# Kernel optimization log

Measured on AMD Instinct MI355X. Metric: run time of the kernel, lower is better.

The kernel has to match this reference:

```python
import jax, jax.numpy as jnp
import numpy as np

ARITY = 8        # children per node (< max_child_number=10, so all children used)
TREE_DEPTH = 5   # internal levels 1..5; depth=5 so GRU applies at every internal node
DIM = 384        # cgf_input_dim == GRU input == GRU hidden (unidirectional, n_layers=1)
VOCAB = 32000


def gru_seq(xs, h0, w_ih, w_hh, b_ih, b_hh):
    # xs: [S, N, D] sequence-major, h0: [N, D]. torch nn.GRU gate order: r, z, n.
    def step(h, x_t):
        gi = x_t @ w_ih.T + b_ih            # [N, 3D]
        gh = h @ w_hh.T + b_hh              # [N, 3D]
        i_r, i_z, i_n = jnp.split(gi, 3, axis=-1)
        h_r, h_z, h_n = jnp.split(gh, 3, axis=-1)
        r = jax.nn.sigmoid(i_r + h_r)
        z = jax.nn.sigmoid(i_z + h_z)
        n = jnp.tanh(i_n + r * h_n)
        h_new = (1.0 - z) * n + z * h
        return h_new, h_new
    h_last, outs = jax.lax.scan(step, h0, xs)
    return outs, h_last                      # [S, N, D], [N, D]


def setup_inputs() -> dict:
    key = jax.random.key(0)
    k1, k2, k3, k4, k5, k6 = jax.random.split(key, 6)
    n_leaves = ARITY ** TREE_DEPTH
    s = 1.0 / np.sqrt(DIM)
    return {
        "leaf_tokens": jax.random.randint(k1, (n_leaves,), 0, VOCAB, dtype=jnp.int32),
        "embed_table": jax.random.normal(k2, (VOCAB, DIM), jnp.float32),
        "w_ih": jax.random.uniform(k3, (3 * DIM, DIM), jnp.float32, -s, s),
        "w_hh": jax.random.uniform(k4, (3 * DIM, DIM), jnp.float32, -s, s),
        "b_ih": jax.random.uniform(k5, (3 * DIM,), jnp.float32, -s, s),
        "b_hh": jax.random.uniform(k6, (3 * DIM,), jnp.float32, -s, s),
    }


def reference(leaf_tokens, embed_table, w_ih, w_hh, b_ih, b_hh):
    # Leaves: embedding-dict lookup -> x=[1,1,D] per leaf; h = zeros.
    x = embed_table[leaf_tokens]             # [A^T, D]
    h = jnp.zeros_like(x)                    # leaf hidden states are zeros
    # Level-synchronous post-order: process deepest internal level first.
    for level in range(TREE_DEPTH, 0, -1):
        n_parents = ARITY ** (level - 1)
        # Children are consumed from last to first (loop i = len-1 .. 0), so
        # the GRU sequence is the REVERSED child order.
        xs = x.reshape(n_parents, ARITY, DIM)[:, ::-1, :].transpose(1, 0, 2)  # [A, P, D]
        h0 = h.reshape(n_parents, ARITY, DIM).mean(axis=1)                     # mean of child hiddens
        outs, h = gru_seq(xs, h0, w_ih, w_hh, b_ih, b_hh)
        x = outs.mean(axis=0)                # mean over the child sequence -> node output [P, D]
    # Root (layer=1) returns res = out of shape [1,1,D]
    return x.reshape(1, 1, DIM)
```

## Files before the change

kernel.cpp:

```cpp
#include <hip/hip_runtime.h>
#include <hip/hip_bf16.h>
#include <stdint.h>

typedef float f32x4 __attribute__((ext_vector_type(4)));
typedef short bf16x8 __attribute__((ext_vector_type(8)));

#define NSLOT 16
#define NDS 24
#define NBLK (NSLOT * NDS)
#define NCTR 788
#define CI(i) ((i) * 32)

__device__ __forceinline__ ushort to_bf16(float f) {
    union { float f; uint32_t u; } v; v.f = f;
    uint32_t u = v.u;
    return (ushort)((u + 0x7fffu + ((u >> 16) & 1u)) >> 16);
}
__device__ __forceinline__ float sigmoid_(float x) { return 1.0f / (1.0f + __expf(-x)); }
__device__ __forceinline__ float tanh_(float x)    { return 1.0f - 2.0f / (__expf(2.0f * x) + 1.0f); }

__device__ __forceinline__ void st_sc1_u16(ushort* p, ushort v) {
    asm volatile("global_store_short %0, %1, off sc1" :: "v"(p), "v"((uint32_t)v) : "memory");
}
__device__ __forceinline__ void st_sc1_f32(float* p, float v) {
    asm volatile("global_store_dword %0, %1, off sc1" :: "v"(p), "v"(v) : "memory");
}
__device__ __forceinline__ void st_sc1_b128(void* p, bf16x8 v) {
    asm volatile("global_store_dwordx4 %0, %1, off sc1" :: "v"(p), "v"(v) : "memory");
}

__global__ void prep_w(const float* __restrict__ w_ih, const float* __restrict__ w_hh,
                       ushort* __restrict__ wswz, unsigned int* __restrict__ ctr) {
    int tid = blockIdx.x * blockDim.x + threadIdx.x;
    if (tid < NCTR * 32) ctr[tid] = 0u;
    if (tid >= 1152 * 96) return;
    int g  = tid / 96;
    int k  = (tid % 96) * 8;
    int kc = k >> 5;
    int q  = (k >> 3) & 3;
    int tile = g >> 4;
    int lane = q * 16 + (g & 15);
    ushort* dst = wswz + ((size_t)(tile * 24 + kc) * 64 + lane) * 8;
    const float* src = (k < 384) ? (w_ih + (size_t)g * 384 + k)
                                 : (w_hh + (size_t)g * 384 + (k - 384));
#pragma unroll
    for (int j = 0; j < 8; ++j) dst[j] = to_bf16(src[j]);
}

__global__ void embed_gather(const int* __restrict__ tok, const float* __restrict__ table,
                             ushort* __restrict__ xleaf, int n_leaves) {
    int tid = blockIdx.x * blockDim.x + threadIdx.x;
    if (tid >= n_leaves * 48) return;
    int leaf = tid / 48, i = tid % 48;
    const float* src = table + (size_t)tok[leaf] * 384 + i * 8;
    bf16x8 v;
#pragma unroll
    for (int j = 0; j < 8; ++j) v[j] = (short)to_bf16(src[j]);
    *(bf16x8*)(xleaf + (size_t)leaf * 384 + i * 8) = v;
}

__device__ __forceinline__ void wait_ge(unsigned int* c, unsigned int n) {
    while (__hip_atomic_fetch_add(c, 0u, __ATOMIC_RELAXED, __HIP_MEMORY_SCOPE_AGENT) < n)
        __builtin_amdgcn_s_sleep(1);
}
__device__ __forceinline__ void wait_ge_coarse(unsigned int* c, unsigned int n) {
    while (__hip_atomic_fetch_add(c, 0u, __ATOMIC_RELAXED, __HIP_MEMORY_SCOPE_AGENT) < n)
        __builtin_amdgcn_s_sleep(127);
}

__device__ __forceinline__ void group_arrive(unsigned int* c) {
    __syncthreads();
    if (threadIdx.x == 0)
        __hip_atomic_fetch_add(c, 1u, __ATOMIC_RELAXED, __HIP_MEMORY_SCOPE_AGENT);
}
__device__ __forceinline__ void group_wait(unsigned int* c) {
    if (threadIdx.x == 0) wait_ge(c, NDS);
    __syncthreads();
}

__device__ __forceinline__ void full_barrier(unsigned int* grpSlot, unsigned int* master) {
    __syncthreads();
    if (threadIdx.x == 0) {
        unsigned int old = __hip_atomic_fetch_add(grpSlot, 1u, __ATOMIC_RELAXED, __HIP_MEMORY_SCOPE_AGENT);
        if (old == NDS - 1)
            __hip_atomic_fetch_add(master, 1u, __ATOMIC_RELAXED, __HIP_MEMORY_SCOPE_AGENT);
        wait_ge_coarse(master, NSLOT);
    }
    __syncthreads();
}

__global__ __launch_bounds__(256, 2)
void tree_gru(const ushort* __restrict__ XA, const ushort* __restrict__ W,
              const float* __restrict__ b_ih, const float* __restrict__ b_hh,
              ushort* __restrict__ HBar, float* __restrict__ Hfar,
              ushort* __restrict__ Xoar,
              unsigned int* __restrict__ ctr, float* __restrict__ out)
{
    __shared__ __align__(16) ushort lw[36864];
    __shared__ __align__(16) ushort stage[4][768];
    const int l = blockIdx.x;
    const int dr = l >> 3;
    const int slot = (l & 7) * 2 + (dr / 24);
    const int ds = dr % 24;
    const int tid = threadIdx.x;
    const int wave = tid >> 6, lane = tid & 63;
    const int quad = lane >> 4, col = lane & 15;
    const int d = ds * 16 + col;

    {
        bf16x8* dstv = (bf16x8*)lw;
#pragma unroll
        for (int g = 0; g < 3; ++g) {
            const bf16x8* s = (const bf16x8*)(W + (size_t)(g * NDS + ds) * 12288);
#pragma unroll
            for (int i = 0; i < 6; ++i) dstv[g * 1536 + i * 256 + tid] = s[i * 256 + tid];
        }
    }
    __syncthreads();

    const float br = b_ih[d] + b_hh[d];
    const float bz = b_ih[384 + d] + b_hh[384 + d];
    const float bi = b_ih[768 + d], bh = b_hh[768 + d];
    const ushort* lwr = &lw[(size_t)lane * 8];

#pragma unroll 1
    for (int lvl = 0; lvl < 5; ++lvl) {
        const int P  = (lvl == 0) ? 4096 : (lvl == 1) ? 512 : (lvl == 2) ? 64 : (lvl == 3) ? 8 : 1;
        const int rp = (lvl == 0) ? 0 : (lvl == 1) ? 4096 : (lvl == 2) ? 4608 : (lvl == 3) ? 4672 : 4680;
        const int rpPrev = (lvl == 1) ? 0 : (lvl == 2) ? 4096 : (lvl == 3) ? 4608 : 4672;
        const int nmp = (P + 31) >> 5;
        const bool leaf = (lvl == 0), root = (lvl == 4);
        const ushort* Xc = leaf ? XA : (Xoar + (size_t)384 * rpPrev);
        const float* Hfprev = leaf ? nullptr : (Hfar + (size_t)384 * rpPrev);
        ushort* HBlvl = HBar + (size_t)9 * 384 * rp;
        ushort* Xout  = Xoar + (size_t)384 * rp;
        float*  Hfout = root ? nullptr : (Hfar + (size_t)384 * rp);
        const size_t N = (size_t)P * 384;
        const bool act = (slot * 4 < nmp);
        if (act) {
            const int mpA = slot * 4 + wave;
            const int mpB = mpA + NSLOT * 4;
            const bool hasA = mpA < nmp;
            const bool hasB = mpB < nmp;
            float hpA[2][4], hsA[2][4], hpB[2][4], hsB[2][4];
#pragma unroll
            for (int mt = 0; mt < 2; ++mt)
#pragma unroll
                for (int r = 0; r < 4; ++r) {
                    hpA[mt][r] = 0.f; hsA[mt][r] = 0.f;
                    hpB[mt][r] = 0.f; hsB[mt][r] = 0.f;
                }
            const f32x4 z4 = (f32x4){0.f, 0.f, 0.f, 0.f};
            const bf16x8 zf = (bf16x8){0, 0, 0, 0, 0, 0, 0, 0};
            struct XA6 { f32x4 r[2], z[2], n[2]; } xA, xB;

            auto xpart = [&](int mp, int child, XA6& o) {
                const int m0 = mp * 32;
                const bool do2 = (m0 + 16) < P;
                const int par0 = m0 + col, par1 = m0 + 16 + col;
                const bool av0 = par0 < P, av1 = par1 < P;
                const ushort* xr0 = Xc + ((size_t)par0 * 8 + child) * 384 + quad * 8;
                const ushort* xr1 = Xc + ((size_t)par1 * 8 + child) * 384 + quad * 8;
                o.r[0] = z4; o.z[0] = z4; o.n[0] = z4;
                o.r[1] = z4; o.z[1] = z4; o.n[1] = z4;
#pragma unroll
                for (int kc = 0; kc < 12; ++kc) {
                    bf16x8 a0 = zf, a1 = zf;
                    if (av0) a0 = *(const bf16x8*)(xr0 + kc * 32);
                    if (do2 && av1) a1 = *(const bf16x8*)(xr1 + kc * 32);
                    bf16x8 bR = *(const bf16x8*)(lwr + kc * 512);
                    bf16x8 bZ = *(const bf16x8*)(lwr + 12288 + kc * 512);
                    bf16x8 bN = *(const bf16x8*)(lwr + 24576 + kc * 512);
                    o.r[0] = __builtin_amdgcn_mfma_f32_16x16x32_bf16(a0, bR, o.r[0], 0, 0, 0);
                    o.z[0] = __builtin_amdgcn_mfma_f32_16x16x32_bf16(a0, bZ, o.z[0], 0, 0, 0);
                    o.n[0] = __builtin_amdgcn_mfma_f32_16x16x32_bf16(a0, bN, o.n[0], 0, 0, 0);
                    if (do2) {
                        o.r[1] = __builtin_amdgcn_mfma_f32_16x16x32_bf16(a1, bR, o.r[1], 0, 0, 0);
                        o.z[1] = __builtin_amdgcn_mfma_f32_16x16x32_bf16(a1, bZ, o.z[1], 0, 0, 0);
                        o.n[1] = __builtin_amdgcn_mfma_f32_16x16x32_bf16(a1, bN, o.n[1], 0, 0, 0);
                    }
                }
            };
            auto prol = [&](int mp, float (&hp)[2][4]) {
                const int m0 = mp * 32;
#pragma unroll
                for (int mt = 0; mt < 2; ++mt)
#pragma unroll
                    for (int r = 0; r < 4; ++r) {
                        const int m = m0 + mt * 16 + quad * 4 + r;
                        if (m < P) {
                            const float* hc = Hfprev + (size_t)m * 8 * 384 + d;
                            float h0 = 0.f;
#pragma unroll
                            for (int c = 0; c < 8; ++c) h0 += hc[(size_t)c * 384];
                            h0 *= 0.125f;
                            hp[mt][r] = h0;
                            st_sc1_u16(&HBlvl[(size_t)m * 384 + d], to_bf16(h0));
                        }
                    }
            };
            auto hpart = [&](int mp, XA6& x, float (&hp)[2][4], float (&hs)[2][4],
                             const ushort* HBp, ushort* HBn, bool hz, bool last) {
                const int m0 = mp * 32;
                const bool do2 = (m0 + 16) < P;
                const int par0 = m0 + col, par1 = m0 + 16 + col;
                const bool av0 = par0 < P, av1 = par1 < P;
                f32x4 n2a = z4, n2b = z4;
                if (!hz) {
                    const ushort* hr0 = HBp + (size_t)par0 * 384 + quad * 8;
                    const ushort* hr1 = HBp + (size_t)par1 * 384 + quad * 8;
#pragma unroll
                    for (int kc = 0; kc < 12; ++kc) {
                        bf16x8 a0 = zf, a1 = zf;
                        if (av0) a0 = *(const bf16x8*)(hr0 + kc * 32);
                        if (do2 && av1) a1 = *(const bf16x8*)(hr1 + kc * 32);
                        bf16x8 bR = *(const bf16x8*)(lwr + (12 + kc) * 512);
                        bf16x8 bZ = *(const bf16x8*)(lwr + 12288 + (12 + kc) * 512);
                        bf16x8 bN = *(const bf16x8*)(lwr + 24576 + (12 + kc) * 512);
                        x.r[0] = __builtin_amdgcn_mfma_f32_16x16x32_bf16(a0, bR, x.r[0], 0, 0, 0);
                        x.z[0] = __builtin_amdgcn_mfma_f32_16x16x32_bf16(a0, bZ, x.z[0], 0, 0, 0);
                        n2a    = __builtin_amdgcn_mfma_f32_16x16x32_bf16(a0, bN, n2a, 0, 0, 0);
                        if (do2) {
                            x.r[1] = __builtin_amdgcn_mfma_f32_16x16x32_bf16(a1, bR, x.r[1], 0, 0, 0);
                            x.z[1] = __builtin_amdgcn_mfma_f32_16x16x32_bf16(a1, bZ, x.z[1], 0, 0, 0);
                            n2b    = __builtin_amdgcn_mfma_f32_16x16x32_bf16(a1, bN, n2b, 0, 0, 0);
                        }
                    }
                }
#pragma unroll
                for (int mt = 0; mt < 2; ++mt) {
                    if (mt && !do2) break;
                    const f32x4 ar = x.r[mt], az = x.z[mt], an1 = x.n[mt];
                    const f32x4 an2 = mt ? n2b : n2a;
#pragma unroll
                    for (int r = 0; r < 4; ++r) {
                        const int m = m0 + mt * 16 + quad * 4 + r;
                        if (m < P) {
                            float rv = sigmoid_(ar[r] + br);
                            float zv = sigmoid_(az[r] + bz);
                            float nv = tanh_(an1[r] + bi + rv * (an2[r] + bh));
                            float hn = (1.0f - zv) * nv + zv * hp[mt][r];
                            hp[mt][r] = hn;
                            hs[mt][r] += hn;
                            if (last) {
                                const size_t idx = (size_t)m * 384 + d;
                                float xo = hs[mt][r] * 0.125f;
                                st_sc1_u16(&Xout[idx], to_bf16(xo));
                                if (!root) st_sc1_f32(&Hfout[idx], hn);
                                else if (m == 0) out[d] = xo;
                            } else {
                                stage[wave][(mt * 16 + quad * 4 + r) * 24 + col] = to_bf16(hn);
                            }
                        }
                    }
                }
                if (!last) {
                    const int row = lane >> 1, half = lane & 1;
                    const int m = m0 + row;
                    if (m < P) {
                        bf16x8 v = *(const bf16x8*)&stage[wave][row * 24 + half * 8];
                        st_sc1_b128(HBn + (size_t)m * 384 + ds * 16 + half * 8, v);
                    }
                }
            };

            if (!leaf) {
                if (hasA) prol(mpA, hpA);
                if (hasB) prol(mpB, hpB);
                group_arrive(&ctr[CI((lvl * 9 + 8) * NSLOT + slot)]);
                if (hasA) xpart(mpA, 7, xA);
                if (hasB) xpart(mpB, 7, xB);
                group_wait(&ctr[CI((lvl * 9 + 8) * NSLOT + slot)]);
            } else {
                if (hasA) xpart(mpA, 7, xA);
                if (hasB) xpart(mpB, 7, xB);
            }
#pragma unroll 1
            for (int t = 0; t < 8; ++t) {
                const ushort* HBp = HBlvl + (size_t)t * N;
                ushort*       HBn = HBlvl + (size_t)(t + 1) * N;
                const bool hz   = leaf && (t == 0);
                const bool last = (t == 7);
                if (hasA) hpart(mpA, xA, hpA, hsA, HBp, HBn, hz, last);
                if (hasB) hpart(mpB, xB, hpB, hsB, HBp, HBn, hz, last);
                if (!last) {
                    unsigned int* c = &ctr[CI((lvl * 9 + t) * NSLOT + slot)];
                    group_arrive(c);
                    const int nchild = 6 - t;
                    if (hasA) xpart(mpA, nchild, xA);
                    if (hasB) xpart(mpB, nchild, xB);
                    group_wait(c);
                }
            }
        }
        if (lvl < 4) full_barrier(&ctr[CI(720 + lvl * NSLOT + slot)], &ctr[CI(784 + lvl)]);
    }
}

extern "C" void kernel_launch(void* const* d_in, const int* in_sizes, int n_in,
                              void* d_out, int out_size, void* d_ws, size_t ws_size,
                              hipStream_t stream) {
    const int*   tok   = (const int*)d_in[0];
    const float* table = (const float*)d_in[1];
    const float* w_ih  = (const float*)d_in[2];
    const float* w_hh  = (const float*)d_in[3];
    const float* b_ih  = (const float*)d_in[4];
    const float* b_hh  = (const float*)d_in[5];
    float* out = (float*)d_out;

    char* ws = (char*)d_ws;
    size_t off = 0;
    auto alloc = [&](size_t bytes) -> void* {
        void* p = ws + off;
        off = (off + bytes + 255) & ~(size_t)255;
        return p;
    };
    ushort* wswz = (ushort*)alloc((size_t)1152 * 768 * 2);
    ushort* XA   = (ushort*)alloc((size_t)32768 * 384 * 2);
    ushort* HBar = (ushort*)alloc((size_t)9 * 4681 * 384 * 2);
    float*  Hfar = (float*)alloc((size_t)4680 * 384 * 4);
    ushort* Xoar = (ushort*)alloc((size_t)4681 * 384 * 2);
    unsigned int* ctr = (unsigned int*)alloc((size_t)NCTR * 32 * 4);

    prep_w<<<(1152 * 96 + 255) / 256, 256, 0, stream>>>(w_ih, w_hh, wswz, ctr);
    embed_gather<<<(32768 * 48 + 255) / 256, 256, 0, stream>>>(tok, table, XA, 32768);
    tree_gru<<<dim3(NBLK), 256, 0, stream>>>(XA, wswz, b_ih, b_hh,
                                             HBar, Hfar, Xoar, ctr, out);
}
```

Before: 624.7 us.

## Probe slot locality at startup and use plain stores when group shares cache

Adds a startup probe in which each block writes a tag and then checks whether the tags of the other blocks in its slot group are visible through normal loads. If every group sees them, the hidden-state exchange stores switch from sc1 write-through stores to ordinary cached stores. The first two full barriers also spin with short sleeps. This trades two extra grid-wide barriers and more counters for cheaper per-step stores, and it relies on the locality probe being a reliable stand-in for cache coherence between blocks.

```diff
diff --git a/kernel.cpp b/kernel.cpp
--- a/kernel.cpp
+++ b/kernel.cpp
@@ -8,7 +8,12 @@
 #define NSLOT 16
 #define NDS 24
 #define NBLK (NSLOT * NDS)
-#define NCTR 788
+#define STEPC(lvl, idx, slot) (((lvl) * 9 + (idx)) * NSLOT + (slot))
+#define FBGC(u, s) (720 + (u) * NSLOT + (s))
+#define FBMC(u)    (816 + (u))
+#define MODEC(s)   (822 + (s))
+#define PROBEC(s, d) (838 + (s) * NDS + (d))
+#define NCTR 1222
 #define CI(i) ((i) * 32)
 
 __device__ __forceinline__ ushort to_bf16(float f) {
@@ -78,13 +83,16 @@
     __syncthreads();
 }
 
-__device__ __forceinline__ void full_barrier(unsigned int* grpSlot, unsigned int* master) {
+__device__ __forceinline__ void full_barrier(unsigned int* ctr, int use, int slot) {
     __syncthreads();
     if (threadIdx.x == 0) {
-        unsigned int old = __hip_atomic_fetch_add(grpSlot, 1u, __ATOMIC_RELAXED, __HIP_MEMORY_SCOPE_AGENT);
+        unsigned int old = __hip_atomic_fetch_add(&ctr[CI(FBGC(use, slot))], 1u,
+                                                  __ATOMIC_RELAXED, __HIP_MEMORY_SCOPE_AGENT);
         if (old == NDS - 1)
-            __hip_atomic_fetch_add(master, 1u, __ATOMIC_RELAXED, __HIP_MEMORY_SCOPE_AGENT);
-        wait_ge_coarse(master, NSLOT);
+            __hip_atomic_fetch_add(&ctr[CI(FBMC(use))], 1u,
+                                   __ATOMIC_RELAXED, __HIP_MEMORY_SCOPE_AGENT);
+        if (use < 2) wait_ge(&ctr[CI(FBMC(use))], NSLOT);
+        else         wait_ge_coarse(&ctr[CI(FBMC(use))], NSLOT);
     }
     __syncthreads();
 }
@@ -98,6 +106,7 @@
 {
     __shared__ __align__(16) ushort lw[36864];
     __shared__ __align__(16) ushort stage[4][768];
+    __shared__ int smode;
     const int l = blockIdx.x;
     const int dr = l >> 3;
     const int slot = (l & 7) * 2 + (dr / 24);
@@ -117,6 +126,28 @@
         }
     }
     __syncthreads();
+
+    if (tid == 0) {
+        *(volatile uint32_t*)&ctr[CI(PROBEC(slot, ds))] =
+            0x5EED0000u | ((uint32_t)slot << 8) | (uint32_t)ds;
+        smode = 0;
+    }
+    full_barrier(ctr, 0, slot);
+    if (tid < NDS) {
+        uint32_t v = *(volatile const uint32_t*)&ctr[CI(PROBEC(slot, tid))];
+        uint32_t expect = 0x5EED0000u | ((uint32_t)slot << 8) | (uint32_t)tid;
+        if (v != expect) atomicOr(&smode, 1);
+    }
+    __syncthreads();
+    if (tid == 0 && smode)
+        __hip_atomic_fetch_or(&ctr[CI(MODEC(slot))], 1u,
+                              __ATOMIC_RELAXED, __HIP_MEMORY_SCOPE_AGENT);
+    full_barrier(ctr, 1, slot);
+    if (tid == 0)
+        smode = (int)__hip_atomic_fetch_add(&ctr[CI(MODEC(slot))], 0u,
+                                            __ATOMIC_RELAXED, __HIP_MEMORY_SCOPE_AGENT);
+    __syncthreads();
+    const bool loc = (smode == 0);
 
     const float br = b_ih[d] + b_hh[d];
     const float bz = b_ih[384 + d] + b_hh[384 + d];
@@ -195,7 +226,9 @@
                             for (int c = 0; c < 8; ++c) h0 += hc[(size_t)c * 384];
                             h0 *= 0.125f;
                             hp[mt][r] = h0;
-                            st_sc1_u16(&HBlvl[(size_t)m * 384 + d], to_bf16(h0));
+                            ushort* p = &HBlvl[(size_t)m * 384 + d];
+                            ushort hv = to_bf16(h0);
+                            if (loc) *p = hv; else st_sc1_u16(p, hv);
                         }
                     }
             };
@@ -259,7 +292,9 @@
                     const int m = m0 + row;
                     if (m < P) {
                         bf16x8 v = *(const bf16x8*)&stage[wave][row * 24 + half * 8];
-                        st_sc1_b128(HBn + (size_t)m * 384 + ds * 16 + half * 8, v);
+                        ushort* p = HBn + (size_t)m * 384 + ds * 16 + half * 8;
+                        if (loc) *(bf16x8*)p = v;
+                        else     st_sc1_b128(p, v);
                     }
                 }
             };
@@ -267,10 +302,10 @@
             if (!leaf) {
                 if (hasA) prol(mpA, hpA);
                 if (hasB) prol(mpB, hpB);
-                group_arrive(&ctr[CI((lvl * 9 + 8) * NSLOT + slot)]);
+                group_arrive(&ctr[CI(STEPC(lvl, 8, slot))]);
                 if (hasA) xpart(mpA, 7, xA);
                 if (hasB) xpart(mpB, 7, xB);
-                group_wait(&ctr[CI((lvl * 9 + 8) * NSLOT + slot)]);
+                group_wait(&ctr[CI(STEPC(lvl, 8, slot))]);
             } else {
                 if (hasA) xpart(mpA, 7, xA);
                 if (hasB) xpart(mpB, 7, xB);
@@ -284,7 +319,7 @@
                 if (hasA) hpart(mpA, xA, hpA, hsA, HBp, HBn, hz, last);
                 if (hasB) hpart(mpB, xB, hpB, hsB, HBp, HBn, hz, last);
                 if (!last) {
-                    unsigned int* c = &ctr[CI((lvl * 9 + t) * NSLOT + slot)];
+                    unsigned int* c = &ctr[CI(STEPC(lvl, t, slot))];
                     group_arrive(c);
                     const int nchild = 6 - t;
                     if (hasA) xpart(mpA, nchild, xA);
@@ -293,7 +328,7 @@
                 }
             }
         }
-        if (lvl < 4) full_barrier(&ctr[CI(720 + lvl * NSLOT + slot)], &ctr[CI(784 + lvl)]);
+        if (lvl < 4) full_barrier(ctr, 2 + lvl, slot);
     }
 }
 
```

New measurement: 631.9 us. No clear change (+1.1%).
